# Kernel tuning notes

Measured on AMD Instinct MI355X. Metric: run time of the kernel, lower is better.

Reference implementation:

```python
import jax, jax.numpy as jnp
import numpy as np

N, L, S, D, H = 2, 2048, 2048, 128, 32  # batch, query len, state len, hidden_dim(=head dim), num_heads


def setup_inputs() -> dict:
    key = jax.random.key(0)
    ks = jax.random.split(key, 8)
    return {
        "query": jax.random.normal(ks[0], (N, L, D), dtype=jnp.float32),
        "states": jax.random.normal(ks[1], (N, S, D), dtype=jnp.float32),
        "Wk": jax.random.normal(ks[2], (H, D, D), dtype=jnp.float32) * 0.05,
        "bk": jax.random.normal(ks[3], (H, D), dtype=jnp.float32) * 0.05,
        "Wv": jax.random.normal(ks[4], (H, D, D), dtype=jnp.float32) * 0.05,
        "bv": jax.random.normal(ks[5], (H, D), dtype=jnp.float32) * 0.05,
        "Wc": jax.random.normal(ks[6], (H * D, D), dtype=jnp.float32) * 0.02,
        "bc": jax.random.normal(ks[7], (D,), dtype=jnp.float32) * 0.02,
    }


def reference(query, states, Wk, bk, Wv, bv, Wc, bc):
    # Per-head key/value projections (Attention.keys_mlp / values_mlp), batched over heads.
    K = jnp.einsum('nsd,hdk->nhsk', states, Wk) + bk[None, :, None, :]  # [N,H,S,D]
    V = jnp.einsum('nsd,hdk->nhsk', states, Wv) + bv[None, :, None, :]  # [N,H,S,D]
    scale = jnp.sqrt(jnp.asarray(K.shape[-1], query.dtype))
    logits = jnp.einsum('nld,nhsd->nhls', query, K) / scale            # [N,H,L,S]
    # Original detaches attention scores (softmax(...).detach()).
    A = jax.lax.stop_gradient(jax.nn.softmax(logits, axis=-1))
    ctx = jnp.einsum('nhls,nhsd->nhld', A, V)                          # [N,H,L,D]
    n, h, l, d = ctx.shape
    ctx = ctx.transpose(0, 2, 1, 3).reshape(n, l, h * d)               # concat heads -> [N,L,H*D]
    return ctx @ Wc + bc                                               # context_transform
```

## Files before the change

kernel.cpp:

```cpp
#include <hip/hip_runtime.h>
#include <hip/hip_bf16.h>

#define N_B 2
#define L_Q 2048
#define S_S 2048
#define D_D 128
#define H_H 32
#define SCALEK (0.08838834764831845f * 1.4426950408889634f)

typedef __attribute__((ext_vector_type(8))) short bf8;
typedef __attribute__((ext_vector_type(4))) short bf4;
typedef __attribute__((ext_vector_type(4))) float f4;

#define MFMA(a, b, c) __builtin_amdgcn_mfma_f32_16x16x32_bf16(a, b, c, 0, 0, 0)

__device__ __forceinline__ short f2bf(float x) {
    union { float f; unsigned u; } v; v.f = x;
    unsigned r = v.u + 0x7FFFu + ((v.u >> 16) & 1u);
    return (short)(r >> 16);
}

__device__ __forceinline__ bf4 pk4(float a, float b, float c, float d) {
    union { __hip_bfloat162 h2[2]; bf4 v; } u;
    u.h2[0] = __float22bfloat162_rn(make_float2(a, b));
    u.h2[1] = __float22bfloat162_rn(make_float2(c, d));
    return u.v;
}

__device__ __forceinline__ bf8 cat44(bf4 lo, bf4 hi) {
    bf8 r;
    r[0] = lo[0]; r[1] = lo[1]; r[2] = lo[2]; r[3] = lo[3];
    r[4] = hi[0]; r[5] = hi[1]; r[6] = hi[2]; r[7] = hi[3];
    return r;
}

__device__ __forceinline__ bf8 load8(const float* p) {
    const float4* q = (const float4*)p;
    float4 a = q[0], b = q[1];
    bf8 r;
    r[0] = f2bf(a.x); r[1] = f2bf(a.y); r[2] = f2bf(a.z); r[3] = f2bf(a.w);
    r[4] = f2bf(b.x); r[5] = f2bf(b.y); r[6] = f2bf(b.z); r[7] = f2bf(b.w);
    return r;
}

__device__ __forceinline__ void async16(const void* g, void* l) {
    __builtin_amdgcn_global_load_lds(
        (const __attribute__((address_space(1))) unsigned*)g,
        (__attribute__((address_space(3))) unsigned*)l, 16, 0, 0);
}

__global__ __launch_bounds__(256) void k_wprep(const float* __restrict__ Wc,
        unsigned short* __restrict__ WcF, const float* __restrict__ Wk,
        const float* __restrict__ Wv, unsigned short* __restrict__ WkF,
        unsigned short* __restrict__ WvF) {
    const int tid = threadIdx.x;
    if (blockIdx.y == 0) {
        int f16 = blockIdx.x * 256 + tid;
        int l = f16 & 63, t = (f16 >> 6) & 3, nfA = (f16 >> 8) & 7, kc = f16 >> 11;
        int lrow = l & 15, lgrp = l >> 4;
        int kbase = kc * 128 + t * 32 + lgrp * 8;
        int n = nfA * 16 + lrow;
        bf8 v;
        #pragma unroll
        for (int j = 0; j < 8; ++j) v[j] = f2bf(Wc[(size_t)(kbase + j) * D_D + n]);
        *(bf8*)(WcF + (size_t)f16 * 8) = v;
        return;
    }
    if (blockIdx.x >= 64) return;
    __shared__ unsigned short T[128][129];
    const int h = blockIdx.x & 31;
    const int job = blockIdx.x >> 5;
    const float* W = (job ? Wv : Wk) + (size_t)h * (D_D * D_D);
    unsigned short* WF = (job ? WvF : WkF) + (size_t)h * (D_D * D_D);

    #pragma unroll
    for (int i = 0; i < 64; ++i) {
        int flat = i * 256 + tid;
        T[flat >> 7][flat & 127] = (unsigned short)f2bf(W[flat]);
    }
    __syncthreads();
    #pragma unroll
    for (int j8 = 0; j8 < 8; ++j8) {
        int f16 = j8 * 256 + tid;
        int l = f16 & 63, t = (f16 >> 6) & 3, df = (f16 >> 8) & 7;
        int lrow = l & 15, lgrp = l >> 4;
        bf8 v;
        #pragma unroll
        for (int j = 0; j < 8; ++j) v[j] = (short)T[t * 32 + lgrp * 8 + j][df * 16 + lrow];
        *(bf8*)(WF + (size_t)f16 * 8) = v;
    }
}

__global__ __launch_bounds__(256) void k_proj(const float* __restrict__ states,
        const unsigned short* __restrict__ WkF, const float* __restrict__ bk,
        const unsigned short* __restrict__ WvF, const float* __restrict__ bv,
        unsigned short* __restrict__ Kb, unsigned short* __restrict__ VTb) {
    const int tid = threadIdx.x;
    const int l = tid & 63, w = tid >> 6;
    const int lrow = l & 15, lgrp = l >> 4;
    const int bx = blockIdx.x;
    const int sc = bx & 31;
    const int nh = bx >> 5;
    const int h = nh & 31, n = nh >> 5;

    const float* srow = states + ((size_t)n * S_S + sc * 64 + w * 16 + lrow) * D_D;
    bf8 sf[4];
    #pragma unroll
    for (int t = 0; t < 4; ++t) sf[t] = load8(srow + t * 32 + lgrp * 8);

    {
        const unsigned short* WF = WkF + (size_t)h * (D_D * D_D);
        f4 acc[8];
        #pragma unroll
        for (int i = 0; i < 8; ++i) acc[i] = (f4)(0.f);
        #pragma unroll
        for (int mf = 0; mf < 8; ++mf) {
            #pragma unroll
            for (int t = 0; t < 4; ++t) {
                bf8 a = *(const bf8*)(WF + (((mf * 4 + t) * 64 + l) << 3));
                acc[mf] = MFMA(a, sf[t], acc[mf]);
            }
        }
        unsigned short* Kout = Kb + (size_t)(n * H_H + h) * S_S * D_D
                                  + (size_t)(sc * 64 + w * 16 + lrow) * D_D;
        #pragma unroll
        for (int mf = 0; mf < 8; ++mf) {
            int d0 = mf * 16 + lgrp * 4;
            float4 bb = *(const float4*)(bk + h * D_D + d0);
            bf4 kv = pk4((acc[mf][0] + bb.x) * SCALEK, (acc[mf][1] + bb.y) * SCALEK,
                         (acc[mf][2] + bb.z) * SCALEK, (acc[mf][3] + bb.w) * SCALEK);
            *(bf4*)(Kout + d0) = kv;
        }
    }
    {
        const unsigned short* WF = WvF + (size_t)h * (D_D * D_D);
        f4 acc[8];
        #pragma unroll
        for (int i = 0; i < 8; ++i) acc[i] = (f4)(0.f);
        #pragma unroll
        for (int nf = 0; nf < 8; ++nf) {
            #pragma unroll
            for (int t = 0; t < 4; ++t) {
                bf8 b = *(const bf8*)(WF + (((nf * 4 + t) * 64 + l) << 3));
                acc[nf] = MFMA(sf[t], b, acc[nf]);
            }
        }
        unsigned short* Vout = VTb + (size_t)(n * H_H + h) * D_D * S_S;
        const int p0 = ((w >> 1) << 5) + (lgrp << 3) + ((w & 1) << 2);
        #pragma unroll
        for (int nf = 0; nf < 8; ++nf) {
            int d = nf * 16 + lrow;
            float bias = bv[h * D_D + d];
            bf4 vv = pk4(acc[nf][0] + bias, acc[nf][1] + bias,
                         acc[nf][2] + bias, acc[nf][3] + bias);
            *(bf4*)(Vout + (size_t)d * S_S + sc * 64 + p0) = vv;
        }
    }
}

__global__ __launch_bounds__(256, 3) void k_attn(const float* __restrict__ query,
        const unsigned short* __restrict__ Kb, const unsigned short* __restrict__ VTb,
        unsigned short* __restrict__ CTX) {
    __shared__ char smem[32768];
    const int tid = threadIdx.x;
    const int l = tid & 63, w = tid >> 6;
    const int lrow = l & 15, lgrp = l >> 4;

    const int bid = blockIdx.x;
    const int bx = (bid & 7) * 128 + (bid >> 3);
    const int qt = bx & 15;
    const int nh = bx >> 4;
    const int h = nh & 31, n = nh >> 5;
    const int qbase = qt * 128 + w * 32;

    bf8 qf[2][4];
    #pragma unroll
    for (int mf = 0; mf < 2; ++mf) {
        const float* qp = query + ((size_t)n * L_Q + qbase + mf * 16 + lrow) * D_D;
        #pragma unroll
        for (int t = 0; t < 4; ++t) qf[mf][t] = load8(qp + t * 32 + lgrp * 8);
    }

    f4 oacc[2][8];
    #pragma unroll
    for (int mf = 0; mf < 2; ++mf)
        #pragma unroll
        for (int df = 0; df < 8; ++df) oacc[mf][df] = (f4)(0.f);
    float rsum[2] = {0.f, 0.f};

    const char* Kg = (const char*)(Kb + (size_t)(n * H_H + h) * S_S * D_D);
    const char* Vg = (const char*)(VTb + (size_t)(n * H_H + h) * D_D * S_S);

    auto stage = [&](int c, int sc2) {
        char* Kl = smem + c * 8192;
        char* Vl = smem + 16384 + c * 8192;
        #pragma unroll
        for (int i = 0; i < 2; ++i) {
            int kop = w * 2 + i;
            int o = kop * 1024 + l * 16;
            int r = o >> 8;
            int b = (o & 255) ^ ((r & 7) << 4);
            async16(Kg + (size_t)(sc2 * 32 + r) * 256 + b, Kl + kop * 1024);
        }
        #pragma unroll
        for (int i = 0; i < 2; ++i) {
            int vop = w * 2 + i;
            int o = vop * 1024 + l * 16;
            int drow = o >> 6;
            int b = (o & 63) ^ (((drow >> 1) & 3) << 4);
            async16(Vg + (size_t)drow * 4096 + sc2 * 64 + b, Vl + vop * 1024);
        }
    };

    auto iter = [&](int cur, int sc2, bool prefetch) {
        if (prefetch) stage(cur ^ 1, sc2 + 1);
        const char* Klds = smem + cur * 8192;
        const char* Vlds = smem + 16384 + cur * 8192;

        f4 sacc[2][2];
        #pragma unroll
        for (int mf = 0; mf < 2; ++mf)
            #pragma unroll
            for (int nf = 0; nf < 2; ++nf) sacc[mf][nf] = (f4)(0.f);
        #pragma unroll
        for (int nf = 0; nf < 2; ++nf) {
            int srow = nf * 16 + lrow;
            int swz = (srow & 7) << 4;
            #pragma unroll
            for (int t = 0; t < 4; ++t) {
                bf8 kb = *(const bf8*)(Klds + srow * 256 + (((t * 32 + lgrp * 8) * 2) ^ swz));
                sacc[0][nf] = MFMA(kb, qf[0][t], sacc[0][nf]);
                sacc[1][nf] = MFMA(kb, qf[1][t], sacc[1][nf]);
            }
        }

        bf8 pf[2];
        #pragma unroll
        for (int mf = 0; mf < 2; ++mf) {
            bf4 pblk[2];
            #pragma unroll
            for (int nf = 0; nf < 2; ++nf) {
                float p0 = __builtin_amdgcn_exp2f(sacc[mf][nf][0]);
                float p1 = __builtin_amdgcn_exp2f(sacc[mf][nf][1]);
                float p2 = __builtin_amdgcn_exp2f(sacc[mf][nf][2]);
                float p3 = __builtin_amdgcn_exp2f(sacc[mf][nf][3]);
                rsum[mf] += (p0 + p1) + (p2 + p3);
                pblk[nf] = pk4(p0, p1, p2, p3);
            }
            pf[mf] = cat44(pblk[0], pblk[1]);
        }

        #pragma unroll
        for (int df = 0; df < 8; ++df) {
            int drow = df * 16 + lrow;
            bf8 vf = *(const bf8*)(Vlds + drow * 64 + ((lgrp * 16) ^ (((drow >> 1) & 3) << 4)));
            oacc[0][df] = MFMA(vf, pf[0], oacc[0][df]);
            oacc[1][df] = MFMA(vf, pf[1], oacc[1][df]);
        }
        __syncthreads();
    };

    stage(0, 0);
    __syncthreads();
    for (int s2 = 0; s2 < 64; s2 += 2) {
        iter(0, s2, true);
        iter(1, s2 + 1, s2 + 1 < 63);
    }

    float rinv[2];
    #pragma unroll
    for (int mf = 0; mf < 2; ++mf) {
        float v = rsum[mf];
        v += __shfl_xor(v, 16, 64);
        v += __shfl_xor(v, 32, 64);
        rinv[mf] = 1.f / v;
    }
    #pragma unroll
    for (int mf = 0; mf < 2; ++mf) {
        int qrow = qbase + mf * 16 + lrow;
        unsigned short* crow = CTX + (size_t)(n * L_Q + qrow) * 4096 + h * D_D;
        #pragma unroll
        for (int df = 0; df < 8; ++df) {
            bf4 o = pk4(oacc[mf][df][0] * rinv[mf], oacc[mf][df][1] * rinv[mf],
                        oacc[mf][df][2] * rinv[mf], oacc[mf][df][3] * rinv[mf]);
            *(bf4*)(crow + df * 16 + lgrp * 4) = o;
        }
    }
}

__global__ __launch_bounds__(256) void k_out(const unsigned short* __restrict__ CTX,
        const unsigned short* __restrict__ WcF, const float* __restrict__ bc,
        float* __restrict__ out) {
    __shared__ char Alds[8192];
    const int tid = threadIdx.x;
    const int l = tid & 63, w = tid >> 6;
    const int lrow = l & 15, lgrp = l >> 4;
    const int m0 = blockIdx.x * 16;
    const char* Ag = (const char*)(CTX + (size_t)m0 * 4096);

    auto stage = [&](int c, int kc) {
        int o = w * 1024 + l * 16;
        int r = o >> 8;
        int b = (o & 255) ^ ((r & 7) << 4);
        async16(Ag + (size_t)r * 8192 + kc * 256 + b, Alds + c * 4096 + w * 1024);
    };

    f4 acc[2];
    acc[0] = (f4)(0.f); acc[1] = (f4)(0.f);
    stage(0, 0);
    __syncthreads();
    int cur = 0;
    for (int kc = 0; kc < 32; ++kc) {
        if (kc < 31) stage(cur ^ 1, kc + 1);
        const char* Ac = Alds + cur * 4096;
        #pragma unroll
        for (int t = 0; t < 4; ++t) {
            int swz = (lrow & 7) << 4;
            bf8 a = *(const bf8*)(Ac + lrow * 256 + (((t * 32 + lgrp * 8) * 2) ^ swz));
            #pragma unroll
            for (int nf = 0; nf < 2; ++nf) {
                int nfA = w * 2 + nf;
                bf8 b = *(const bf8*)(WcF + ((size_t)(((kc * 8 + nfA) * 4 + t) * 64 + l) << 3));
                acc[nf] = MFMA(a, b, acc[nf]);
            }
        }
        __syncthreads();
        cur ^= 1;
    }
    #pragma unroll
    for (int nf = 0; nf < 2; ++nf) {
        int nc = w * 32 + nf * 16 + lrow;
        float bias = bc[nc];
        #pragma unroll
        for (int r = 0; r < 4; ++r)
            out[(size_t)(m0 + lgrp * 4 + r) * D_D + nc] = acc[nf][r] + bias;
    }
}

extern "C" void kernel_launch(void* const* d_in, const int* in_sizes, int n_in,
                              void* d_out, int out_size, void* d_ws, size_t ws_size,
                              hipStream_t stream) {
    const float* query  = (const float*)d_in[0];
    const float* states = (const float*)d_in[1];
    const float* Wk = (const float*)d_in[2];
    const float* bk = (const float*)d_in[3];
    const float* Wv = (const float*)d_in[4];
    const float* bv = (const float*)d_in[5];
    const float* Wc = (const float*)d_in[6];
    const float* bc = (const float*)d_in[7];
    float* out = (float*)d_out;

    char* ws = (char*)d_ws;
    unsigned short* Kb  = (unsigned short*)(ws);
    unsigned short* VTb = (unsigned short*)(ws + 33554432);
    unsigned short* CTX = (unsigned short*)(ws + 67108864);
    unsigned short* WkF = (unsigned short*)(ws + 67108864);
    unsigned short* WvF = (unsigned short*)(ws + 67108864 + 1048576);
    unsigned short* WcF = (unsigned short*)(ws + 100663296);

    dim3 gp(256, 2);
    k_wprep<<<gp, 256, 0, stream>>>(Wc, WcF, Wk, Wv, WkF, WvF);
    k_proj<<<2048, 256, 0, stream>>>(states, WkF, bk, WvF, bv, Kb, VTb);
    k_attn<<<1024, 256, 0, stream>>>(query, Kb, VTb, CTX);
    k_out<<<256, 256, 0, stream>>>(CTX, WcF, bc, out);
}
```

Baseline: 218.4 us.

## Restructure attention into single-wave blocks with pre-tiled V and 16x16x16 MFMA

```diff
diff --git a/kernel.cpp b/kernel.cpp
--- a/kernel.cpp
+++ b/kernel.cpp
@@ -14,6 +14,18 @@
 
 #define MFMA(a, b, c) __builtin_amdgcn_mfma_f32_16x16x32_bf16(a, b, c, 0, 0, 0)
 
+#if defined(__HIP_DEVICE_COMPILE__)
+# if __has_builtin(__builtin_amdgcn_mfma_f32_16x16x16bf16_1k)
+#  define MFMA16(a, b, c) __builtin_amdgcn_mfma_f32_16x16x16bf16_1k(a, b, c, 0, 0, 0)
+# elif __has_builtin(__builtin_amdgcn_mfma_f32_16x16x16_bf16)
+#  define MFMA16(a, b, c) __builtin_amdgcn_mfma_f32_16x16x16_bf16(a, b, c, 0, 0, 0)
+# else
+#  error "no 16x16x16 bf16 mfma builtin on device"
+# endif
+#else
+# define MFMA16(a, b, c) (c)
+#endif
+
 __device__ __forceinline__ short f2bf(float x) {
     union { float f; unsigned u; } v; v.f = x;
     unsigned r = v.u + 0x7FFFu + ((v.u >> 16) & 1u);
@@ -25,13 +37,6 @@
     u.h2[0] = __float22bfloat162_rn(make_float2(a, b));
     u.h2[1] = __float22bfloat162_rn(make_float2(c, d));
     return u.v;
-}
-
-__device__ __forceinline__ bf8 cat44(bf4 lo, bf4 hi) {
-    bf8 r;
-    r[0] = lo[0]; r[1] = lo[1]; r[2] = lo[2]; r[3] = lo[3];
-    r[4] = hi[0]; r[5] = hi[1]; r[6] = hi[2]; r[7] = hi[3];
-    return r;
 }
 
 __device__ __forceinline__ bf8 load8(const float* p) {
@@ -121,7 +126,7 @@
                 acc[mf] = MFMA(a, sf[t], acc[mf]);
             }
         }
-        unsigned short* Kout = Kb + (size_t)(n * H_H + h) * S_S * D_D
+        unsigned short* Kout = Kb + (size_t)nh * S_S * D_D
                                   + (size_t)(sc * 64 + w * 16 + lrow) * D_D;
         #pragma unroll
         for (int mf = 0; mf < 8; ++mf) {
@@ -145,33 +150,33 @@
                 acc[nf] = MFMA(sf[t], b, acc[nf]);
             }
         }
-        unsigned short* Vout = VTb + (size_t)(n * H_H + h) * D_D * S_S;
-        const int p0 = ((w >> 1) << 5) + (lgrp << 3) + ((w & 1) << 2);
+        unsigned short* vbase = VTb + (size_t)nh * (D_D * S_S)
+                                    + (size_t)(sc * 4 + w) * 2048;
+        const int so = lrow * 16 + 4 * (lgrp ^ ((lrow >> 2) & 3));
         #pragma unroll
         for (int nf = 0; nf < 8; ++nf) {
             int d = nf * 16 + lrow;
             float bias = bv[h * D_D + d];
             bf4 vv = pk4(acc[nf][0] + bias, acc[nf][1] + bias,
                          acc[nf][2] + bias, acc[nf][3] + bias);
-            *(bf4*)(Vout + (size_t)d * S_S + sc * 64 + p0) = vv;
-        }
-    }
-}
-
-__global__ __launch_bounds__(256, 3) void k_attn(const float* __restrict__ query,
+            *(bf4*)(vbase + nf * 256 + so) = vv;
+        }
+    }
+}
+
+__global__ __launch_bounds__(64, 3) void k_attn(const float* __restrict__ query,
         const unsigned short* __restrict__ Kb, const unsigned short* __restrict__ VTb,
         unsigned short* __restrict__ CTX) {
-    __shared__ char smem[32768];
-    const int tid = threadIdx.x;
-    const int l = tid & 63, w = tid >> 6;
+    __shared__ char smem[16384];
+    const int l = threadIdx.x & 63;
     const int lrow = l & 15, lgrp = l >> 4;
 
     const int bid = blockIdx.x;
-    const int bx = (bid & 7) * 128 + (bid >> 3);
-    const int qt = bx & 15;
-    const int nh = bx >> 4;
+    const int bx = (bid & 7) * 512 + (bid >> 3);
+    const int qt = bx & 63;
+    const int nh = bx >> 6;
     const int h = nh & 31, n = nh >> 5;
-    const int qbase = qt * 128 + w * 32;
+    const int qbase = qt * 32;
 
     bf8 qf[2][4];
     #pragma unroll
@@ -188,83 +193,70 @@
         for (int df = 0; df < 8; ++df) oacc[mf][df] = (f4)(0.f);
     float rsum[2] = {0.f, 0.f};
 
-    const char* Kg = (const char*)(Kb + (size_t)(n * H_H + h) * S_S * D_D);
-    const char* Vg = (const char*)(VTb + (size_t)(n * H_H + h) * D_D * S_S);
-
-    auto stage = [&](int c, int sc2) {
-        char* Kl = smem + c * 8192;
-        char* Vl = smem + 16384 + c * 8192;
-        #pragma unroll
-        for (int i = 0; i < 2; ++i) {
-            int kop = w * 2 + i;
-            int o = kop * 1024 + l * 16;
+    const char* Kg = (const char*)(Kb + (size_t)nh * S_S * D_D);
+    const char* Vg = (const char*)(VTb + (size_t)nh * D_D * S_S);
+
+    auto stage = [&](int c, int i) {
+        char* Kl = smem + c * 4096;
+        char* Vl = smem + 8192 + c * 4096;
+        #pragma unroll
+        for (int j = 0; j < 4; ++j) {
+            int o = j * 1024 + l * 16;
             int r = o >> 8;
             int b = (o & 255) ^ ((r & 7) << 4);
-            async16(Kg + (size_t)(sc2 * 32 + r) * 256 + b, Kl + kop * 1024);
-        }
-        #pragma unroll
-        for (int i = 0; i < 2; ++i) {
-            int vop = w * 2 + i;
-            int o = vop * 1024 + l * 16;
-            int drow = o >> 6;
-            int b = (o & 63) ^ (((drow >> 1) & 3) << 4);
-            async16(Vg + (size_t)drow * 4096 + sc2 * 64 + b, Vl + vop * 1024);
-        }
+            async16(Kg + (size_t)(i * 16 + r) * 256 + b, Kl + j * 1024);
+        }
+        #pragma unroll
+        for (int j = 0; j < 4; ++j)
+            async16(Vg + (size_t)i * 4096 + j * 1024 + l * 16, Vl + j * 1024);
     };
 
-    auto iter = [&](int cur, int sc2, bool prefetch) {
-        if (prefetch) stage(cur ^ 1, sc2 + 1);
-        const char* Klds = smem + cur * 8192;
-        const char* Vlds = smem + 16384 + cur * 8192;
-
-        f4 sacc[2][2];
-        #pragma unroll
-        for (int mf = 0; mf < 2; ++mf)
-            #pragma unroll
-            for (int nf = 0; nf < 2; ++nf) sacc[mf][nf] = (f4)(0.f);
-        #pragma unroll
-        for (int nf = 0; nf < 2; ++nf) {
-            int srow = nf * 16 + lrow;
-            int swz = (srow & 7) << 4;
-            #pragma unroll
-            for (int t = 0; t < 4; ++t) {
-                bf8 kb = *(const bf8*)(Klds + srow * 256 + (((t * 32 + lgrp * 8) * 2) ^ swz));
-                sacc[0][nf] = MFMA(kb, qf[0][t], sacc[0][nf]);
-                sacc[1][nf] = MFMA(kb, qf[1][t], sacc[1][nf]);
-            }
-        }
-
-        bf8 pf[2];
+    const int kswz = (lrow & 7) << 4;
+    const int voff = lrow * 32 + 8 * (lgrp ^ ((lrow >> 2) & 3));
+
+    auto iter = [&](int cur, int i) {
+        if (i + 1 < 128) {
+            stage(cur ^ 1, i + 1);
+            asm volatile("s_waitcnt vmcnt(8)" ::: "memory");
+        } else {
+            asm volatile("s_waitcnt vmcnt(0)" ::: "memory");
+        }
+        __builtin_amdgcn_sched_barrier(0);
+        const char* Klds = smem + cur * 4096;
+        const char* Vlds = smem + 8192 + cur * 4096;
+
+        f4 sacc[2];
+        sacc[0] = (f4)(0.f); sacc[1] = (f4)(0.f);
+        #pragma unroll
+        for (int t = 0; t < 4; ++t) {
+            bf8 kb = *(const bf8*)(Klds + lrow * 256 + ((t * 64 + lgrp * 16) ^ kswz));
+            sacc[0] = MFMA(kb, qf[0][t], sacc[0]);
+            sacc[1] = MFMA(kb, qf[1][t], sacc[1]);
+        }
+
+        bf4 pf[2];
         #pragma unroll
         for (int mf = 0; mf < 2; ++mf) {
-            bf4 pblk[2];
-            #pragma unroll
-            for (int nf = 0; nf < 2; ++nf) {
-                float p0 = __builtin_amdgcn_exp2f(sacc[mf][nf][0]);
-                float p1 = __builtin_amdgcn_exp2f(sacc[mf][nf][1]);
-                float p2 = __builtin_amdgcn_exp2f(sacc[mf][nf][2]);
-                float p3 = __builtin_amdgcn_exp2f(sacc[mf][nf][3]);
-                rsum[mf] += (p0 + p1) + (p2 + p3);
-                pblk[nf] = pk4(p0, p1, p2, p3);
-            }
-            pf[mf] = cat44(pblk[0], pblk[1]);
+            float p0 = __builtin_amdgcn_exp2f(sacc[mf][0]);
+            float p1 = __builtin_amdgcn_exp2f(sacc[mf][1]);
+            float p2 = __builtin_amdgcn_exp2f(sacc[mf][2]);
+            float p3 = __builtin_amdgcn_exp2f(sacc[mf][3]);
+            rsum[mf] += (p0 + p1) + (p2 + p3);
+            pf[mf] = pk4(p0, p1, p2, p3);
         }
 
         #pragma unroll
         for (int df = 0; df < 8; ++df) {
-            int drow = df * 16 + lrow;
-            bf8 vf = *(const bf8*)(Vlds + drow * 64 + ((lgrp * 16) ^ (((drow >> 1) & 3) << 4)));
-            oacc[0][df] = MFMA(vf, pf[0], oacc[0][df]);
-            oacc[1][df] = MFMA(vf, pf[1], oacc[1][df]);
-        }
-        __syncthreads();
+            bf4 vf = *(const bf4*)(Vlds + df * 512 + voff);
+            oacc[0][df] = MFMA16(vf, pf[0], oacc[0][df]);
+            oacc[1][df] = MFMA16(vf, pf[1], oacc[1][df]);
+        }
     };
 
     stage(0, 0);
-    __syncthreads();
-    for (int s2 = 0; s2 < 64; s2 += 2) {
-        iter(0, s2, true);
-        iter(1, s2 + 1, s2 + 1 < 63);
+    for (int i = 0; i < 128; i += 2) {
+        iter(0, i);
+        iter(1, i + 1);
     }
 
     float rinv[2];
@@ -361,6 +353,6 @@
     dim3 gp(256, 2);
     k_wprep<<<gp, 256, 0, stream>>>(Wc, WcF, Wk, Wv, WkF, WvF);
     k_proj<<<2048, 256, 0, stream>>>(states, WkF, bk, WvF, bv, Kb, VTb);
-    k_attn<<<1024, 256, 0, stream>>>(query, Kb, VTb, CTX);
+    k_attn<<<4096, 64, 0, stream>>>(query, Kb, VTb, CTX);
     k_out<<<256, 256, 0, stream>>>(CTX, WcF, bc, out);
 }
```

Result: slower. 284.8 us (+30.4%).
